# Optimization experiments

Measured on AMD Instinct MI355X. Metric: run time of the kernel, lower is better.

Reference implementation:

```python
import jax, jax.numpy as jnp
import numpy as np

D, H, C = 256, 512, 128  # input_size, hidden_size, num_classes


def setup_inputs() -> dict:
    key = jax.random.key(0)
    ks = jax.random.split(key, 10)
    s_in = 1.0 / np.sqrt(H)  # torch Linear init scale (out_features=H)
    inp = {
        "x": jax.random.normal(ks[0], (512, 64, D), dtype=jnp.float32),
        "h0": jnp.zeros((2, 64, H), dtype=jnp.float32),
        "c0": jnp.zeros((2, 64, H), dtype=jnp.float32),
        # gate order along 4H axis: i, f, o, c
        "W0": jax.random.uniform(ks[1], (4 * H, D), jnp.float32, -s_in, s_in),
        "U0": jax.random.uniform(ks[2], (4 * H, H), jnp.float32, -s_in, s_in),
        "b0": jax.random.uniform(ks[3], (4 * H,), jnp.float32, -s_in, s_in),
        "W1": jax.random.uniform(ks[4], (4 * H, H), jnp.float32, -s_in, s_in),
        "U1": jax.random.uniform(ks[5], (4 * H, H), jnp.float32, -s_in, s_in),
        "b1": jax.random.uniform(ks[6], (4 * H,), jnp.float32, -s_in, s_in),
        "fc_w": jax.random.uniform(ks[7], (C, H), jnp.float32, -s_in, s_in),
        "fc_b": jax.random.uniform(ks[8], (C,), jnp.float32, -s_in, s_in),
    }
    return inp


def _cell(xt, h, c, W, U, b):
    # fused gate projection: equivalent to 8 separate Linears (W_*, U_*) concatenated
    g = xt @ W.T + h @ U.T + b  # [N, 4H]
    i, f, o, ct = jnp.split(g, 4, axis=-1)
    i = jax.nn.sigmoid(i)
    f = jax.nn.sigmoid(f)
    o = jax.nn.sigmoid(o)
    ct = jnp.tanh(ct)
    c_new = f * c + i * ct
    h_new = o * jnp.tanh(c_new)
    return h_new, c_new


def reference(x, h0, c0, W0, U0, b0, W1, U1, b1, fc_w, fc_b):
    def step(carry, xt):
        h_a, c_a, h_b, c_b = carry
        h_a, c_a = _cell(xt, h_a, c_a, W0, U0, b0)
        h_b, c_b = _cell(h_a, h_b, c_b, W1, U1, b1)
        return (h_a, c_a, h_b, c_b), h_b

    carry0 = (h0[0], c0[0], h0[1], c0[1])
    (h_a, c_a, h_b, c_b), out_seq = jax.lax.scan(step, carry0, x)
    out = out_seq[-1] @ fc_w.T + fc_b  # last time step -> [N, C]
    h_n = jnp.stack([h_a, h_b])
    c_n = jnp.stack([c_a, c_b])
    return out, h_n, c_n
```

## Files before the change

### kernel.cpp

```cpp
#include <hip/hip_runtime.h>
#include <hip/hip_fp16.h>

typedef _Float16 f16;
typedef _Float16 f16x8 __attribute__((ext_vector_type(8)));
typedef float f32x4 __attribute__((ext_vector_type(4)));

#define TT 512

#define XH_OFF    0
#define WP_OFF    16777216
#define HA_OFF    24117248
#define HB_OFF    24379392
#define BAR_OFF   24510464
#define WS_NEED   24510976

#define WP_L1_HOFF 1572864
#define LDS_BYTES 131072

#define WAITV(N) do { \
    asm volatile("s_waitcnt vmcnt(" #N ")" ::: "memory"); \
    __builtin_amdgcn_sched_barrier(0); \
  } while (0)


__global__ void k_pack_w(const float* __restrict__ W0, const float* __restrict__ U0,
                         const float* __restrict__ W1, const float* __restrict__ U1,
                         f16* __restrict__ wp) {
  int idx = blockIdx.x * 256 + threadIdx.x;
  if (idx >= 458752) return;
  if (idx < 196608) {
    int w = idx / 6144, r = idx % 6144;
    int ct = r / 1536, r2 = r % 1536;
    int s = r2 / 64, lane = r2 % 64;
    int g = ct * 512 + w * 16 + (lane & 15);
    int kb = s * 32 + (lane >> 4) * 8;
    f16* dst = wp + (size_t)idx * 8;
#pragma unroll
    for (int j = 0; j < 8; ++j) {
      int k = kb + j;
      float v = (k < 256) ? W0[g * 256 + k] : U0[g * 512 + (k - 256)];
      dst[j] = (f16)v;
    }
  } else {
    int i2 = idx - 196608;
    int w = i2 / 8192, r = i2 % 8192;
    int ct = r / 2048, r2 = r % 2048;
    int s = r2 / 64, lane = r2 % 64;
    int g = ct * 512 + w * 16 + (lane & 15);
    int kb = s * 32 + (lane >> 4) * 8;
    f16* dst = wp + (size_t)WP_L1_HOFF + (size_t)i2 * 8;
#pragma unroll
    for (int j = 0; j < 8; ++j) {
      int k = kb + j;
      float v = (k < 512) ? W1[g * 512 + k] : U1[g * 512 + (k - 512)];
      dst[j] = (f16)v;
    }
  }
}

__global__ void k_pack_x(const float* __restrict__ x, f16* __restrict__ xh) {
  int t = blockIdx.x * 256 + threadIdx.x;
  if (t >= 1048576) return;
  const float4* s = (const float4*)(x) + (size_t)t * 2;
  float4 a = s[0], b = s[1];
  f16x8 o;
  o[0] = (f16)a.x; o[1] = (f16)a.y; o[2] = (f16)a.z; o[3] = (f16)a.w;
  o[4] = (f16)b.x; o[5] = (f16)b.y; o[6] = (f16)b.z; o[7] = (f16)b.w;
  *(f16x8*)(xh + (size_t)t * 8) = o;
}

__global__ void k_init(const float* __restrict__ h0, f16* __restrict__ ha,
                       f16* __restrict__ hb, int* __restrict__ slots) {
  int i = blockIdx.x * 256 + threadIdx.x;
  if (i < 32768) {
    ha[i] = (f16)h0[i];
  } else if (i < 65536) {
    hb[i] = (f16)h0[i];
  }
  if (i < 66) slots[i] = 0;
}


__device__ __forceinline__ float sigmoidf_(float x) {
  return 1.0f / (1.0f + __expf(-x));
}
__device__ __forceinline__ float tanhf_(float x) {
  x = fminf(fmaxf(x, -15.0f), 15.0f);
  float e = __expf(-2.0f * x);
  return (1.0f - e) / (1.0f + e);
}

__device__ __forceinline__ uint4 ldg_coh(const void* base, unsigned voff) {
  uint4 d;
  asm volatile("global_load_dwordx4 %0, %1, %2 sc0 sc1"
               : "=v"(d) : "v"(voff), "s"(base) : "memory");
  return d;
}
__device__ __forceinline__ uint4 ldg_x(const void* base, unsigned voff) {
  uint4 d;
  asm volatile("global_load_dwordx4 %0, %1, %2"
               : "=v"(d) : "v"(voff), "s"(base) : "memory");
  return d;
}


template <int LAYER>
__device__ void lstm_body(const f16* __restrict__ xh, const f16* __restrict__ wp,
                          f16* __restrict__ ha, f16* __restrict__ hb,
                          int* __restrict__ slots, const float* __restrict__ c0,
                          const float* __restrict__ bb, float* __restrict__ dout,
                          f16* lds) {
  constexpr int NX = (LAYER == 0) ? 8 : 0;
  constexpr int NH = (LAYER == 0) ? 16 : 32;
  constexpr int NK = NX + NH;
  const int wg = blockIdx.x;
  const int w = wg & 31;
  const int tid = threadIdx.x, lane = tid & 63, wv = tid >> 6;
  int* gens = slots + 64;

  {
    const uint4* src = (const uint4*)(wp + (LAYER ? (size_t)WP_L1_HOFF + (size_t)w * 65536
                                                  : (size_t)w * 49152));
    uint4* dst = (uint4*)lds;
    const int n16 = LAYER ? 8192 : 6144;
    for (int i = tid; i < n16; i += 256) dst[i] = src[i];
  }

  const int j15 = lane & 15;
  const int l4 = lane >> 4;
  const int hidb = w * 16 + j15;
  const float bi = bb[hidb], bf = bb[512 + hidb], bo = bb[1024 + hidb], bc = bb[1536 + hidb];

  float cr[4];
#pragma unroll
  for (int r = 0; r < 4; ++r) {
    int n = 16 * wv + l4 * 4 + r;
    cr[r] = c0[(size_t)LAYER * 32768 + n * 512 + hidb];
  }

  const int row = 16 * wv + j15;
  const unsigned hoffs = (unsigned)(row * 1024 + l4 * 16);
  const unsigned xoffs = (unsigned)(row * 512 + l4 * 16);

  uint4 ax[(LAYER == 0) ? 8 : 1];
  uint4 ah[NH];

  auto issue_x = [&](int pp) {
    if constexpr (LAYER == 0) {
      const char* xb = (const char*)xh + (size_t)pp * 32768;
#pragma unroll
      for (int s = 0; s < 8; ++s) ax[s] = ldg_x(xb, xoffs + s * 64);
    }
  };

  __syncthreads();
  issue_x(0);

  bool broken = false;
  for (int p = 0; p <= TT; ++p) {
    const char* hard = (const char*)ha + (size_t)(p & 3) * 65536;
    const char* hbrd = (const char*)hb + (size_t)(p & 1) * 65536;
    f16* hwr = (LAYER == 0) ? (ha + ((p + 1) & 3) * 32768)
                            : (hb + (((p & 1) ^ 1) * 32768));
    const bool active = (LAYER == 0) ? (p < TT) : (p >= 1);

    if (active) {
      f32x4 acc[4];
#pragma unroll
      for (int ct = 0; ct < 4; ++ct) acc[ct] = (f32x4){0.f, 0.f, 0.f, 0.f};

      auto mstep = [&](uint4 Au, int sB) {
        f16x8 a = __builtin_bit_cast(f16x8, Au);
#pragma unroll
        for (int ct = 0; ct < 4; ++ct) {
          f16x8 b = *(const f16x8*)(lds + (((ct * NK + sB) * 64 + lane) * 8));
          acc[ct] = __builtin_amdgcn_mfma_f32_16x16x32_f16(a, b, acc[ct], 0, 0, 0);
        }
      };

      if constexpr (LAYER == 0) {
#pragma unroll
        for (int t = 0; t < 16; ++t) ah[t] = ldg_coh(hard, hoffs + t * 64);
        WAITV(16);
#pragma unroll
        for (int s = 0; s < 8; ++s) mstep(ax[s], s);
        WAITV(8);
#pragma unroll
        for (int t = 0; t < 8; ++t) mstep(ah[t], 8 + t);
        WAITV(0);
#pragma unroll
        for (int t = 8; t < 16; ++t) mstep(ah[t], 8 + t);
      } else {
#pragma unroll
        for (int t = 0; t < 16; ++t) ah[t] = ldg_coh(hard, hoffs + t * 64);
        WAITV(8);
#pragma unroll
        for (int t = 0; t < 8; ++t) mstep(ah[t], t);
#pragma unroll
        for (int t = 16; t < 24; ++t) ah[t] = ldg_coh(hbrd, hoffs + (t - 16) * 64);
        WAITV(8);
#pragma unroll
        for (int t = 8; t < 16; ++t) mstep(ah[t], t);
#pragma unroll
        for (int t = 24; t < 32; ++t) ah[t] = ldg_coh(hbrd, hoffs + (t - 16) * 64);
        WAITV(8);
#pragma unroll
        for (int t = 16; t < 24; ++t) mstep(ah[t], t);
        WAITV(0);
#pragma unroll
        for (int t = 24; t < 32; ++t) mstep(ah[t], t);
      }

      const bool last = (p == (LAYER ? TT : TT - 1));
#pragma unroll
      for (int r = 0; r < 4; ++r) {
        int n = 16 * wv + l4 * 4 + r;
        float gi = acc[0][r] + bi;
        float gf = acc[1][r] + bf;
        float go = acc[2][r] + bo;
        float gc = acc[3][r] + bc;
        float ig = sigmoidf_(gi), fg = sigmoidf_(gf), og = sigmoidf_(go);
        float cg = tanhf_(gc);
        float c = fg * cr[r] + ig * cg;
        cr[r] = c;
        float h = og * tanhf_(c);
        unsigned short us = __builtin_bit_cast(unsigned short, (f16)h);
        unsigned other = __shfl_xor((unsigned)us, 1, 64);
        if (!(lane & 1)) {
          unsigned pack = (unsigned)us | (other << 16);
          __hip_atomic_store((unsigned*)(hwr + n * 512 + hidb), pack,
                             __ATOMIC_RELAXED, __HIP_MEMORY_SCOPE_AGENT);
        }
        if (last) {
          dout[8192 + LAYER * 32768 + n * 512 + hidb] = h;
          dout[73728 + LAYER * 32768 + n * 512 + hidb] = c;
        }
      }
    }

    WAITV(0);
    __builtin_amdgcn_s_barrier();
    if (tid == 0)
      __hip_atomic_store(slots + wg, p + 1, __ATOMIC_RELAXED, __HIP_MEMORY_SCOPE_AGENT);
    if constexpr (LAYER == 0) {
      if (p + 1 < TT) issue_x(p + 1);
    }
    if (p < TT && wv == 0 && !broken) {
      const int tgt = p + 1;
      if (w == 0) {
        const int* gs = slots + (LAYER ? 32 : 0);
        unsigned spins = 0;
        for (;;) {
          int v = __hip_atomic_load(gs + (lane & 31), __ATOMIC_RELAXED,
                                    __HIP_MEMORY_SCOPE_AGENT);
          if (__all((int)(v >= tgt))) break;
          __builtin_amdgcn_s_sleep(1);
          if (++spins > (1u << 20)) { broken = true; break; }
        }
        __hip_atomic_store(gens + LAYER, tgt, __ATOMIC_RELAXED, __HIP_MEMORY_SCOPE_AGENT);
        const int needO = LAYER ? tgt : (p - 1);
        if (needO > 0 && !broken) {
          spins = 0;
          for (;;) {
            int o = __hip_atomic_load(gens + (1 - LAYER), __ATOMIC_RELAXED,
                                      __HIP_MEMORY_SCOPE_AGENT);
            if (o >= needO) break;
            __builtin_amdgcn_s_sleep(2);
            if (++spins > (1u << 20)) { broken = true; break; }
          }
        }
      } else {
        const int need1 = LAYER ? tgt : (p - 1);
        unsigned spins = 0;
        for (;;) {
          unsigned long long g = __hip_atomic_load((const unsigned long long*)gens,
                                                   __ATOMIC_RELAXED,
                                                   __HIP_MEMORY_SCOPE_AGENT);
          int g0 = (int)(unsigned)g, g1 = (int)(unsigned)(g >> 32);
          if (g0 >= tgt && g1 >= need1) break;
          __builtin_amdgcn_s_sleep(2);
          if (++spins > (1u << 20)) { broken = true; break; }
        }
      }
    }
    __builtin_amdgcn_s_barrier();
  }
}

__global__ __launch_bounds__(256, 1) void k_lstm(const f16* __restrict__ xh,
                                                 const f16* __restrict__ wp,
                                                 f16* __restrict__ ha, f16* __restrict__ hb,
                                                 int* __restrict__ slots,
                                                 const float* __restrict__ c0,
                                                 const float* __restrict__ b0,
                                                 const float* __restrict__ b1,
                                                 float* __restrict__ dout) {
  extern __shared__ f16 lds[];
  if (blockIdx.x < 32) lstm_body<0>(xh, wp, ha, hb, slots, c0, b0, dout, lds);
  else                 lstm_body<1>(xh, wp, ha, hb, slots, c0, b1, dout, lds);
}


__global__ void k_fc(const float* __restrict__ hn1, const float* __restrict__ fcw,
                     const float* __restrict__ fcb, float* __restrict__ out) {
  int n = blockIdx.x, cc = threadIdx.x;
  const float* h = hn1 + n * 512;
  const float* wr = fcw + cc * 512;
  float s = fcb[cc];
#pragma unroll 4
  for (int k = 0; k < 512; k += 4) {
    float4 hv = *(const float4*)(h + k);
    float4 wv = *(const float4*)(wr + k);
    s += hv.x * wv.x + hv.y * wv.y + hv.z * wv.z + hv.w * wv.w;
  }
  out[n * 128 + cc] = s;
}


extern "C" void kernel_launch(void* const* d_in, const int* in_sizes, int n_in,
                              void* d_out, int out_size, void* d_ws, size_t ws_size,
                              hipStream_t stream) {
  const float* x   = (const float*)d_in[0];
  const float* h0  = (const float*)d_in[1];
  const float* c0  = (const float*)d_in[2];
  const float* W0  = (const float*)d_in[3];
  const float* U0  = (const float*)d_in[4];
  const float* b0  = (const float*)d_in[5];
  const float* W1  = (const float*)d_in[6];
  const float* U1  = (const float*)d_in[7];
  const float* b1  = (const float*)d_in[8];
  const float* fcw = (const float*)d_in[9];
  const float* fcb = (const float*)d_in[10];
  float* out = (float*)d_out;
  char* ws = (char*)d_ws;
  if (ws_size < (size_t)WS_NEED) return;

  f16* xh = (f16*)(ws + XH_OFF);
  f16* wp = (f16*)(ws + WP_OFF);
  f16* ha = (f16*)(ws + HA_OFF);
  f16* hb = (f16*)(ws + HB_OFF);
  int* slots = (int*)(ws + BAR_OFF);

  (void)hipFuncSetAttribute((const void*)k_lstm,
                            hipFuncAttributeMaxDynamicSharedMemorySize, LDS_BYTES);

  k_pack_w<<<(458752 + 255) / 256, 256, 0, stream>>>(W0, U0, W1, U1, wp);
  k_pack_x<<<(1048576 + 255) / 256, 256, 0, stream>>>(x, xh);
  k_init<<<256, 256, 0, stream>>>(h0, ha, hb, slots);
  k_lstm<<<64, 256, LDS_BYTES, stream>>>(xh, wp, ha, hb, slots, c0, b0, b1, out);
  k_fc<<<64, 128, 0, stream>>>(out + 8192 + 32768, fcw, fcb, out);
}
```

Measured before the change: 3.673 ms.

## Split grid barrier into per-wave generation waits with early h loads

```diff
diff --git a/kernel.cpp b/kernel.cpp
--- a/kernel.cpp
+++ b/kernel.cpp
@@ -165,6 +165,40 @@
     const bool active = (LAYER == 0) ? (p < TT) : (p >= 1);
 
     if (active) {
+      {
+        bool ownOk = false, othOk = false;
+        const int needOth = (LAYER == 0) ? (p - 2) : p;
+        unsigned spins = 0;
+        for (;;) {
+          unsigned long long g = __hip_atomic_load((const unsigned long long*)gens,
+                                                   __ATOMIC_RELAXED,
+                                                   __HIP_MEMORY_SCOPE_AGENT);
+          const int g0 = (int)(unsigned)g, g1 = (int)(unsigned)(g >> 32);
+          const int gown = LAYER ? g1 : g0;
+          const int goth = LAYER ? g0 : g1;
+          if (!ownOk && gown >= p) {
+            ownOk = true;
+            if constexpr (LAYER == 0) {
+#pragma unroll
+              for (int t = 0; t < 16; ++t) ah[t] = ldg_coh(hard, hoffs + t * 64);
+            } else {
+#pragma unroll
+              for (int t = 0; t < 16; ++t) ah[t] = ldg_coh(hbrd, hoffs + t * 64);
+            }
+          }
+          if (ownOk && !othOk && goth >= needOth) {
+            othOk = true;
+            if constexpr (LAYER == 1) {
+#pragma unroll
+              for (int t = 0; t < 16; ++t) ah[16 + t] = ldg_coh(hard, hoffs + t * 64);
+            }
+          }
+          if (ownOk && othOk) break;
+          __builtin_amdgcn_s_sleep(1);
+          if (++spins > (1u << 20)) { broken = true; break; }
+        }
+      }
+
       f32x4 acc[4];
 #pragma unroll
       for (int ct = 0; ct < 4; ++ct) acc[ct] = (f32x4){0.f, 0.f, 0.f, 0.f};
@@ -179,8 +213,6 @@
       };
 
       if constexpr (LAYER == 0) {
-#pragma unroll
-        for (int t = 0; t < 16; ++t) ah[t] = ldg_coh(hard, hoffs + t * 64);
         WAITV(16);
 #pragma unroll
         for (int s = 0; s < 8; ++s) mstep(ax[s], s);
@@ -191,24 +223,18 @@
 #pragma unroll
         for (int t = 8; t < 16; ++t) mstep(ah[t], 8 + t);
       } else {
-#pragma unroll
-        for (int t = 0; t < 16; ++t) ah[t] = ldg_coh(hard, hoffs + t * 64);
+        WAITV(24);
+#pragma unroll
+        for (int t = 0; t < 8; ++t) mstep(ah[t], 16 + t);
+        WAITV(16);
+#pragma unroll
+        for (int t = 8; t < 16; ++t) mstep(ah[t], 16 + t);
         WAITV(8);
 #pragma unroll
-        for (int t = 0; t < 8; ++t) mstep(ah[t], t);
-#pragma unroll
-        for (int t = 16; t < 24; ++t) ah[t] = ldg_coh(hbrd, hoffs + (t - 16) * 64);
-        WAITV(8);
-#pragma unroll
-        for (int t = 8; t < 16; ++t) mstep(ah[t], t);
-#pragma unroll
-        for (int t = 24; t < 32; ++t) ah[t] = ldg_coh(hbrd, hoffs + (t - 16) * 64);
-        WAITV(8);
-#pragma unroll
-        for (int t = 16; t < 24; ++t) mstep(ah[t], t);
+        for (int t = 0; t < 8; ++t) mstep(ah[16 + t], t);
         WAITV(0);
 #pragma unroll
-        for (int t = 24; t < 32; ++t) mstep(ah[t], t);
+        for (int t = 8; t < 16; ++t) mstep(ah[16 + t], t);
       }
 
       const bool last = (p == (LAYER ? TT : TT - 1));
@@ -238,16 +264,15 @@
       }
     }
 
-    WAITV(0);
-    __builtin_amdgcn_s_barrier();
-    if (tid == 0)
-      __hip_atomic_store(slots + wg, p + 1, __ATOMIC_RELAXED, __HIP_MEMORY_SCOPE_AGENT);
-    if constexpr (LAYER == 0) {
+    if (p < TT) {
+      WAITV(0);
+      __builtin_amdgcn_s_barrier();
+      if (tid == 0)
+        __hip_atomic_store(slots + wg, p + 1, __ATOMIC_RELAXED,
+                           __HIP_MEMORY_SCOPE_AGENT);
       if (p + 1 < TT) issue_x(p + 1);
-    }
-    if (p < TT && wv == 0 && !broken) {
-      const int tgt = p + 1;
-      if (w == 0) {
+      if (w == 0 && wv == 0 && !broken) {
+        const int tgt = p + 1;
         const int* gs = slots + (LAYER ? 32 : 0);
         unsigned spins = 0;
         for (;;) {
@@ -257,33 +282,10 @@
           __builtin_amdgcn_s_sleep(1);
           if (++spins > (1u << 20)) { broken = true; break; }
         }
-        __hip_atomic_store(gens + LAYER, tgt, __ATOMIC_RELAXED, __HIP_MEMORY_SCOPE_AGENT);
-        const int needO = LAYER ? tgt : (p - 1);
-        if (needO > 0 && !broken) {
-          spins = 0;
-          for (;;) {
-            int o = __hip_atomic_load(gens + (1 - LAYER), __ATOMIC_RELAXED,
-                                      __HIP_MEMORY_SCOPE_AGENT);
-            if (o >= needO) break;
-            __builtin_amdgcn_s_sleep(2);
-            if (++spins > (1u << 20)) { broken = true; break; }
-          }
-        }
-      } else {
-        const int need1 = LAYER ? tgt : (p - 1);
-        unsigned spins = 0;
-        for (;;) {
-          unsigned long long g = __hip_atomic_load((const unsigned long long*)gens,
-                                                   __ATOMIC_RELAXED,
-                                                   __HIP_MEMORY_SCOPE_AGENT);
-          int g0 = (int)(unsigned)g, g1 = (int)(unsigned)(g >> 32);
-          if (g0 >= tgt && g1 >= need1) break;
-          __builtin_amdgcn_s_sleep(2);
-          if (++spins > (1u << 20)) { broken = true; break; }
-        }
+        __hip_atomic_store(gens + LAYER, tgt, __ATOMIC_RELAXED,
+                           __HIP_MEMORY_SCOPE_AGENT);
       }
     }
-    __builtin_amdgcn_s_barrier();
   }
 }
 
```

Result: slower. 4.067 ms (+10.7%).

## Use per-step hidden-state buffers to drop coherent loads and cross-layer waits

Applied to the files above, without the earlier changes.

```diff
diff --git a/kernel.cpp b/kernel.cpp
--- a/kernel.cpp
+++ b/kernel.cpp
@@ -9,10 +9,10 @@
 
 #define XH_OFF    0
 #define WP_OFF    16777216
-#define HA_OFF    24117248
-#define HB_OFF    24379392
-#define BAR_OFF   24510464
-#define WS_NEED   24510976
+#define BAR_OFF   24117248
+#define HA_OFF    24118272
+#define HB_OFF    57738240
+#define WS_NEED   91423744
 
 #define WP_L1_HOFF 1572864
 #define LDS_BYTES 131072
@@ -70,14 +70,25 @@
 }
 
 __global__ void k_init(const float* __restrict__ h0, f16* __restrict__ ha,
-                       f16* __restrict__ hb, int* __restrict__ slots) {
+                       f16* __restrict__ hb, int* __restrict__ bar) {
   int i = blockIdx.x * 256 + threadIdx.x;
-  if (i < 32768) {
-    ha[i] = (f16)h0[i];
-  } else if (i < 65536) {
-    hb[i] = (f16)h0[i];
-  }
-  if (i < 66) slots[i] = 0;
+  if (i < 16384) {
+    int n = i >> 8, k2 = (i & 255) * 2;
+    unsigned short a = __builtin_bit_cast(unsigned short, (f16)h0[n * 512 + k2]);
+    unsigned short b = __builtin_bit_cast(unsigned short, (f16)h0[n * 512 + k2 + 1]);
+    unsigned pack = (unsigned)a | ((unsigned)b << 16);
+    __hip_atomic_store((unsigned*)(ha + n * 512 + k2), pack,
+                       __ATOMIC_RELAXED, __HIP_MEMORY_SCOPE_AGENT);
+  } else if (i < 32768) {
+    int j = i - 16384;
+    int n = j >> 8, k2 = (j & 255) * 2;
+    unsigned short a = __builtin_bit_cast(unsigned short, (f16)h0[32768 + n * 512 + k2]);
+    unsigned short b = __builtin_bit_cast(unsigned short, (f16)h0[32768 + n * 512 + k2 + 1]);
+    unsigned pack = (unsigned)a | ((unsigned)b << 16);
+    __hip_atomic_store((unsigned*)(hb + 32768 + n * 512 + k2), pack,
+                       __ATOMIC_RELAXED, __HIP_MEMORY_SCOPE_AGENT);
+  }
+  if (i < 130) bar[i] = 0;
 }
 
 
@@ -90,12 +101,6 @@
   return (1.0f - e) / (1.0f + e);
 }
 
-__device__ __forceinline__ uint4 ldg_coh(const void* base, unsigned voff) {
-  uint4 d;
-  asm volatile("global_load_dwordx4 %0, %1, %2 sc0 sc1"
-               : "=v"(d) : "v"(voff), "s"(base) : "memory");
-  return d;
-}
 __device__ __forceinline__ uint4 ldg_x(const void* base, unsigned voff) {
   uint4 d;
   asm volatile("global_load_dwordx4 %0, %1, %2"
@@ -107,7 +112,7 @@
 template <int LAYER>
 __device__ void lstm_body(const f16* __restrict__ xh, const f16* __restrict__ wp,
                           f16* __restrict__ ha, f16* __restrict__ hb,
-                          int* __restrict__ slots, const float* __restrict__ c0,
+                          int* __restrict__ bar, const float* __restrict__ c0,
                           const float* __restrict__ bb, float* __restrict__ dout,
                           f16* lds) {
   constexpr int NX = (LAYER == 0) ? 8 : 0;
@@ -116,7 +121,9 @@
   const int wg = blockIdx.x;
   const int w = wg & 31;
   const int tid = threadIdx.x, lane = tid & 63, wv = tid >> 6;
-  int* gens = slots + 64;
+  int* pslots = bar;
+  int* slots = bar + 64;
+  int* gens = bar + 128;
 
   {
     const uint4* src = (const uint4*)(wp + (LAYER ? (size_t)WP_L1_HOFF + (size_t)w * 65536
@@ -138,6 +145,24 @@
     cr[r] = c0[(size_t)LAYER * 32768 + n * 512 + hidb];
   }
 
+  __syncthreads();
+  if (tid == 0) {
+    __threadfence();
+    __hip_atomic_store(pslots + wg, 1, __ATOMIC_RELAXED, __HIP_MEMORY_SCOPE_AGENT);
+  }
+  bool broken = false;
+  if (wv == 0) {
+    unsigned spins = 0;
+    for (;;) {
+      int v = __hip_atomic_load(pslots + lane, __ATOMIC_RELAXED,
+                                __HIP_MEMORY_SCOPE_AGENT);
+      if (__all((int)(v >= 1))) break;
+      __builtin_amdgcn_s_sleep(1);
+      if (++spins > (1u << 22)) { broken = true; break; }
+    }
+  }
+  __syncthreads();
+
   const int row = 16 * wv + j15;
   const unsigned hoffs = (unsigned)(row * 1024 + l4 * 16);
   const unsigned xoffs = (unsigned)(row * 512 + l4 * 16);
@@ -152,16 +177,12 @@
       for (int s = 0; s < 8; ++s) ax[s] = ldg_x(xb, xoffs + s * 64);
     }
   };
-
-  __syncthreads();
   issue_x(0);
 
-  bool broken = false;
   for (int p = 0; p <= TT; ++p) {
-    const char* hard = (const char*)ha + (size_t)(p & 3) * 65536;
-    const char* hbrd = (const char*)hb + (size_t)(p & 1) * 65536;
-    f16* hwr = (LAYER == 0) ? (ha + ((p + 1) & 3) * 32768)
-                            : (hb + (((p & 1) ^ 1) * 32768));
+    const char* hard = (const char*)ha + (size_t)p * 65536;
+    const char* hbrd = (const char*)hb + (size_t)p * 65536;
+    f16* hwr = ((LAYER == 0) ? ha : hb) + (size_t)(p + 1) * 32768;
     const bool active = (LAYER == 0) ? (p < TT) : (p >= 1);
 
     if (active) {
@@ -180,7 +201,7 @@
 
       if constexpr (LAYER == 0) {
 #pragma unroll
-        for (int t = 0; t < 16; ++t) ah[t] = ldg_coh(hard, hoffs + t * 64);
+        for (int t = 0; t < 16; ++t) ah[t] = ldg_x(hard, hoffs + t * 64);
         WAITV(16);
 #pragma unroll
         for (int s = 0; s < 8; ++s) mstep(ax[s], s);
@@ -192,17 +213,15 @@
         for (int t = 8; t < 16; ++t) mstep(ah[t], 8 + t);
       } else {
 #pragma unroll
-        for (int t = 0; t < 16; ++t) ah[t] = ldg_coh(hard, hoffs + t * 64);
-        WAITV(8);
+        for (int t = 0; t < 16; ++t) ah[t] = ldg_x(hard, hoffs + t * 64);
+#pragma unroll
+        for (int t = 0; t < 16; ++t) ah[16 + t] = ldg_x(hbrd, hoffs + t * 64);
+        WAITV(24);
 #pragma unroll
         for (int t = 0; t < 8; ++t) mstep(ah[t], t);
-#pragma unroll
-        for (int t = 16; t < 24; ++t) ah[t] = ldg_coh(hbrd, hoffs + (t - 16) * 64);
-        WAITV(8);
+        WAITV(16);
 #pragma unroll
         for (int t = 8; t < 16; ++t) mstep(ah[t], t);
-#pragma unroll
-        for (int t = 24; t < 32; ++t) ah[t] = ldg_coh(hbrd, hoffs + (t - 16) * 64);
         WAITV(8);
 #pragma unroll
         for (int t = 16; t < 24; ++t) mstep(ah[t], t);
@@ -238,66 +257,67 @@
       }
     }
 
-    WAITV(0);
-    __builtin_amdgcn_s_barrier();
-    if (tid == 0)
-      __hip_atomic_store(slots + wg, p + 1, __ATOMIC_RELAXED, __HIP_MEMORY_SCOPE_AGENT);
-    if constexpr (LAYER == 0) {
-      if (p + 1 < TT) issue_x(p + 1);
-    }
-    if (p < TT && wv == 0 && !broken) {
-      const int tgt = p + 1;
-      if (w == 0) {
-        const int* gs = slots + (LAYER ? 32 : 0);
-        unsigned spins = 0;
-        for (;;) {
-          int v = __hip_atomic_load(gs + (lane & 31), __ATOMIC_RELAXED,
-                                    __HIP_MEMORY_SCOPE_AGENT);
-          if (__all((int)(v >= tgt))) break;
-          __builtin_amdgcn_s_sleep(1);
-          if (++spins > (1u << 20)) { broken = true; break; }
-        }
-        __hip_atomic_store(gens + LAYER, tgt, __ATOMIC_RELAXED, __HIP_MEMORY_SCOPE_AGENT);
-        const int needO = LAYER ? tgt : (p - 1);
-        if (needO > 0 && !broken) {
-          spins = 0;
+    if (p < TT) {
+      WAITV(0);
+      __builtin_amdgcn_s_barrier();
+      if (tid == 0)
+        __hip_atomic_store(slots + wg, p + 1, __ATOMIC_RELAXED,
+                           __HIP_MEMORY_SCOPE_AGENT);
+      if constexpr (LAYER == 0) {
+        if (p + 1 < TT) issue_x(p + 1);
+      }
+      if (wv == 0 && !broken) {
+        const int tgt = p + 1;
+        if (w == 0) {
+          const int* gs = slots + (LAYER ? 32 : 0);
+          unsigned spins = 0;
           for (;;) {
-            int o = __hip_atomic_load(gens + (1 - LAYER), __ATOMIC_RELAXED,
+            int v = __hip_atomic_load(gs + (lane & 31), __ATOMIC_RELAXED,
                                       __HIP_MEMORY_SCOPE_AGENT);
-            if (o >= needO) break;
+            if (__all((int)(v >= tgt))) break;
+            __builtin_amdgcn_s_sleep(1);
+            if (++spins > (1u << 20)) { broken = true; break; }
+          }
+          __hip_atomic_store(gens + LAYER, tgt, __ATOMIC_RELAXED,
+                             __HIP_MEMORY_SCOPE_AGENT);
+          if (LAYER == 1 && !broken) {
+            unsigned s2 = 0;
+            while (__hip_atomic_load(gens, __ATOMIC_RELAXED,
+                                     __HIP_MEMORY_SCOPE_AGENT) < tgt) {
+              __builtin_amdgcn_s_sleep(2);
+              if (++s2 > (1u << 20)) { broken = true; break; }
+            }
+          }
+        } else {
+          unsigned spins = 0;
+          for (;;) {
+            unsigned long long g = __hip_atomic_load((const unsigned long long*)gens,
+                                                     __ATOMIC_RELAXED,
+                                                     __HIP_MEMORY_SCOPE_AGENT);
+            int g0 = (int)(unsigned)g, g1 = (int)(unsigned)(g >> 32);
+            bool ok = (LAYER == 0) ? (g0 >= tgt) : (g0 >= tgt && g1 >= tgt);
+            if (ok) break;
             __builtin_amdgcn_s_sleep(2);
             if (++spins > (1u << 20)) { broken = true; break; }
           }
         }
-      } else {
-        const int need1 = LAYER ? tgt : (p - 1);
-        unsigned spins = 0;
-        for (;;) {
-          unsigned long long g = __hip_atomic_load((const unsigned long long*)gens,
-                                                   __ATOMIC_RELAXED,
-                                                   __HIP_MEMORY_SCOPE_AGENT);
-          int g0 = (int)(unsigned)g, g1 = (int)(unsigned)(g >> 32);
-          if (g0 >= tgt && g1 >= need1) break;
-          __builtin_amdgcn_s_sleep(2);
-          if (++spins > (1u << 20)) { broken = true; break; }
-        }
       }
-    }
-    __builtin_amdgcn_s_barrier();
+      __builtin_amdgcn_s_barrier();
+    }
   }
 }
 
 __global__ __launch_bounds__(256, 1) void k_lstm(const f16* __restrict__ xh,
                                                  const f16* __restrict__ wp,
                                                  f16* __restrict__ ha, f16* __restrict__ hb,
-                                                 int* __restrict__ slots,
+                                                 int* __restrict__ bar,
                                                  const float* __restrict__ c0,
                                                  const float* __restrict__ b0,
                                                  const float* __restrict__ b1,
                                                  float* __restrict__ dout) {
   extern __shared__ f16 lds[];
-  if (blockIdx.x < 32) lstm_body<0>(xh, wp, ha, hb, slots, c0, b0, dout, lds);
-  else                 lstm_body<1>(xh, wp, ha, hb, slots, c0, b1, dout, lds);
+  if (blockIdx.x < 32) lstm_body<0>(xh, wp, ha, hb, bar, c0, b0, dout, lds);
+  else                 lstm_body<1>(xh, wp, ha, hb, bar, c0, b1, dout, lds);
 }
 
 
@@ -337,16 +357,16 @@
 
   f16* xh = (f16*)(ws + XH_OFF);
   f16* wp = (f16*)(ws + WP_OFF);
+  int* bar = (int*)(ws + BAR_OFF);
   f16* ha = (f16*)(ws + HA_OFF);
   f16* hb = (f16*)(ws + HB_OFF);
-  int* slots = (int*)(ws + BAR_OFF);
 
   (void)hipFuncSetAttribute((const void*)k_lstm,
                             hipFuncAttributeMaxDynamicSharedMemorySize, LDS_BYTES);
 
   k_pack_w<<<(458752 + 255) / 256, 256, 0, stream>>>(W0, U0, W1, U1, wp);
   k_pack_x<<<(1048576 + 255) / 256, 256, 0, stream>>>(x, xh);
-  k_init<<<256, 256, 0, stream>>>(h0, ha, hb, slots);
-  k_lstm<<<64, 256, LDS_BYTES, stream>>>(xh, wp, ha, hb, slots, c0, b0, b1, out);
+  k_init<<<128, 256, 0, stream>>>(h0, ha, hb, bar);
+  k_lstm<<<64, 256, LDS_BYTES, stream>>>(xh, wp, ha, hb, bar, c0, b0, b1, out);
   k_fc<<<64, 128, 0, stream>>>(out + 8192 + 32768, fcw, fcb, out);
 }
```

Result: slower. 4.225 ms (+15.0%).

## Replace two-level generation barrier with per-block direct slot polling and LDS flag

Applied to the files above, without the earlier changes.

```diff
diff --git a/kernel.cpp b/kernel.cpp
--- a/kernel.cpp
+++ b/kernel.cpp
@@ -15,7 +15,7 @@
 #define WS_NEED   24510976
 
 #define WP_L1_HOFF 1572864
-#define LDS_BYTES 131072
+#define LDS_BYTES 131136
 
 #define WAITV(N) do { \
     asm volatile("s_waitcnt vmcnt(" #N ")" ::: "memory"); \
@@ -77,7 +77,7 @@
   } else if (i < 65536) {
     hb[i] = (f16)h0[i];
   }
-  if (i < 66) slots[i] = 0;
+  if (i < 64) slots[i] = 0;
 }
 
 
@@ -116,7 +116,7 @@
   const int wg = blockIdx.x;
   const int w = wg & 31;
   const int tid = threadIdx.x, lane = tid & 63, wv = tid >> 6;
-  int* gens = slots + 64;
+  volatile int* lflag = (volatile int*)(lds + 65536);
 
   {
     const uint4* src = (const uint4*)(wp + (LAYER ? (size_t)WP_L1_HOFF + (size_t)w * 65536
@@ -125,6 +125,7 @@
     const int n16 = LAYER ? 8192 : 6144;
     for (int i = tid; i < n16; i += 256) dst[i] = src[i];
   }
+  if (tid == 0) *lflag = 0;
 
   const int j15 = lane & 15;
   const int l4 = lane >> 4;
@@ -238,52 +239,46 @@
       }
     }
 
-    WAITV(0);
-    __builtin_amdgcn_s_barrier();
-    if (tid == 0)
-      __hip_atomic_store(slots + wg, p + 1, __ATOMIC_RELAXED, __HIP_MEMORY_SCOPE_AGENT);
-    if constexpr (LAYER == 0) {
-      if (p + 1 < TT) issue_x(p + 1);
-    }
-    if (p < TT && wv == 0 && !broken) {
+    if (p < TT) {
+      WAITV(0);
+      __builtin_amdgcn_s_barrier();
+      if (tid == 0)
+        __hip_atomic_store(slots + wg, p + 1, __ATOMIC_RELAXED,
+                           __HIP_MEMORY_SCOPE_AGENT);
+      if constexpr (LAYER == 0) {
+        if (p + 1 < TT) issue_x(p + 1);
+      }
       const int tgt = p + 1;
-      if (w == 0) {
-        const int* gs = slots + (LAYER ? 32 : 0);
-        unsigned spins = 0;
-        for (;;) {
-          int v = __hip_atomic_load(gs + (lane & 31), __ATOMIC_RELAXED,
-                                    __HIP_MEMORY_SCOPE_AGENT);
-          if (__all((int)(v >= tgt))) break;
-          __builtin_amdgcn_s_sleep(1);
-          if (++spins > (1u << 20)) { broken = true; break; }
-        }
-        __hip_atomic_store(gens + LAYER, tgt, __ATOMIC_RELAXED, __HIP_MEMORY_SCOPE_AGENT);
-        const int needO = LAYER ? tgt : (p - 1);
-        if (needO > 0 && !broken) {
-          spins = 0;
+      if (wv == 0) {
+        if (!broken) {
+          unsigned spins = 0;
           for (;;) {
-            int o = __hip_atomic_load(gens + (1 - LAYER), __ATOMIC_RELAXED,
+            int v = __hip_atomic_load(slots + lane, __ATOMIC_RELAXED,
                                       __HIP_MEMORY_SCOPE_AGENT);
-            if (o >= needO) break;
+            unsigned long long bT = __ballot(v >= tgt);
+            bool ok;
+            if (LAYER == 0) {
+              unsigned long long bR = __ballot(v >= p - 1);
+              ok = ((bT & 0xFFFFFFFFull) == 0xFFFFFFFFull) &&
+                   ((bR >> 32) == 0xFFFFFFFFull);
+            } else {
+              ok = (bT == ~0ull);
+            }
+            if (ok) break;
             __builtin_amdgcn_s_sleep(2);
             if (++spins > (1u << 20)) { broken = true; break; }
           }
         }
+        __builtin_amdgcn_sched_barrier(0);
+        if (lane == 0) *lflag = tgt;
       } else {
-        const int need1 = LAYER ? tgt : (p - 1);
         unsigned spins = 0;
-        for (;;) {
-          unsigned long long g = __hip_atomic_load((const unsigned long long*)gens,
-                                                   __ATOMIC_RELAXED,
-                                                   __HIP_MEMORY_SCOPE_AGENT);
-          int g0 = (int)(unsigned)g, g1 = (int)(unsigned)(g >> 32);
-          if (g0 >= tgt && g1 >= need1) break;
-          __builtin_amdgcn_s_sleep(2);
-          if (++spins > (1u << 20)) { broken = true; break; }
+        while (*lflag < tgt) {
+          __builtin_amdgcn_s_sleep(1);
+          if (++spins > (1u << 24)) break;
         }
       }
     }
-    __builtin_amdgcn_s_barrier();
   }
 }
 
```

Measured after the change: 4.064 ms. 10.6% more time.
